# Kernel tuning notes

Measured on AMD Instinct MI355X. Metric: run time of the kernel, lower is better.

Reference implementation:

```python
import jax, jax.numpy as jnp
import numpy as np

N, E = 50000, 800000
IN, H, D, K = 256, 4, 64, 3
NEG_SLOPE = 0.2

def leaky_relu(x):
    return jnp.where(x >= 0, x, NEG_SLOPE * x)

def setup_inputs() -> dict:
    key = jax.random.key(0)
    ks = jax.random.split(key, 10)
    feat = jax.random.normal(ks[0], (N, IN), dtype=jnp.float32)
    src = jax.random.randint(ks[1], (E,), 0, N)
    dst = jax.random.randint(ks[2], (E,), 0, N)
    g = np.sqrt(2.0)  # relu gain used by xavier init; scale irrelevant to math
    W_src = jax.random.normal(ks[3], (H * D, IN), dtype=jnp.float32) * (g * np.sqrt(2.0 / (IN + H * D)))
    attn_l = jax.random.normal(ks[4], (1, H, D), dtype=jnp.float32) * 0.1
    attn_r = jax.random.normal(ks[5], (1, H, D), dtype=jnp.float32) * 0.1
    hop_attn_l = jax.random.normal(ks[6], (1, H, D), dtype=jnp.float32) * 0.1
    hop_attn_r = jax.random.normal(ks[7], (1, H, D), dtype=jnp.float32) * 0.1
    pos_emb = jax.random.normal(ks[8], (1, H, K + 1, D), dtype=jnp.float32) * 0.1
    bias = jnp.zeros((H * D,), dtype=jnp.float32)
    return {"feat": feat, "src": src, "dst": dst, "W_src": W_src,
            "attn_l": attn_l, "attn_r": attn_r, "hop_attn_l": hop_attn_l,
            "hop_attn_r": hop_attn_r, "pos_emb": pos_emb, "bias": bias}

def edge_softmax_dst(e, dst):
    # e: [E, H], softmax over incoming edges of each dst node
    m = jax.ops.segment_max(e, dst, num_segments=N)          # [N, H]
    m = jnp.where(jnp.isfinite(m), m, 0.0)                   # empty segments
    ex = jnp.exp(e - m[dst])                                 # [E, H]
    s = jax.ops.segment_sum(ex, dst, num_segments=N)         # [N, H]
    denom = s[dst]
    return jnp.where(denom > 0, ex / denom, 0.0)

def reference(feat, src, dst, W_src, attn_l, attn_r, hop_attn_l, hop_attn_r, pos_emb, bias):
    # fc_src (shared with fc_dst): [N, IN] -> [N, H, D]
    feat_src = (feat @ W_src.T).reshape(N, H, D)
    feat_dst = feat_src  # share_weights=True
    # GAT transition matrix, norm_by='dst'
    el = jnp.sum(feat_src * attn_l, axis=-1)   # [N, H]
    er = jnp.sum(feat_dst * attn_r, axis=-1)   # [N, H]
    e = leaky_relu(el[src] + er[dst])          # [E, H]
    a = edge_softmax_dst(e, dst)               # [E, H]
    # K-hop diffusion with positional embedding per hop
    h = feat_src
    hstack = [h + pos_emb[:, :, 0, :]]
    for k in range(1, K + 1):
        msg = a[:, :, None] * h[src]                          # [E, H, D]
        h = jax.ops.segment_sum(msg, dst, num_segments=N)     # [N, H, D]
        hstack.append(h + pos_emb[:, :, k, :])
    hs = jnp.stack(hstack, axis=2)                            # [N, H, K+1, D]
    # Hop-wise attention (HA)
    a_l = jnp.sum(hs * hop_attn_l[:, :, None, :], axis=-1, keepdims=True)            # [N,H,K+1,1]
    a_r = jnp.sum(hs[:, :, :1, :] * hop_attn_r[:, :, None, :], axis=-1, keepdims=True)  # [N,H,1,1]
    hop_a = jax.nn.softmax(leaky_relu(a_l + a_r), axis=2)
    rst = jnp.sum(hs * hop_a, axis=2)                         # [N, H, D]
    rst = rst + bias.reshape(1, H, D)
    return rst
```

## Files before the change

### kernel.cpp

```cpp
#include <hip/hip_runtime.h>
#include <hip/hip_bf16.h>
#include <hip/hip_fp16.h>

#define NN 50000
#define EE 800000
#define INF_ 256
#define HH 4
#define DD 64
#define KK 3
#define NEG_SLOPE 0.2f

struct __align__(8) half4 { __half2 a, b; };

__device__ __forceinline__ float lrelu(float x) {
    return x >= 0.0f ? x : NEG_SLOPE * x;
}

__device__ __forceinline__ float wave_sum(float v) {
    #pragma unroll
    for (int m = 1; m < 64; m <<= 1) v += __shfl_xor(v, m, 64);
    return v;
}

__global__ __launch_bounds__(256) void gemm_fs(const float* __restrict__ A,
                                               const float* __restrict__ W,
                                               const float* __restrict__ al,
                                               const float* __restrict__ ar,
                                               float* __restrict__ C,
                                               __half* __restrict__ C16,
                                               float* __restrict__ el,
                                               float* __restrict__ er, int M) {
    const int K = INF_;
    __shared__ float As[16][68];
    __shared__ float Bs[16][68];
    int tid = threadIdx.x;
    int tx = tid & 15, ty = tid >> 4;
    int m0 = blockIdx.y * 64;
    int j0 = blockIdx.x * 64;
    int lrow = tid >> 2;
    int lcol4 = (tid & 3) * 4;
    float c[4][4] = {};
    for (int k0 = 0; k0 < K; k0 += 16) {
        float4 av = make_float4(0.f, 0.f, 0.f, 0.f);
        if (m0 + lrow < M) av = *(const float4*)&A[(size_t)(m0 + lrow) * K + k0 + lcol4];
        float4 bv = *(const float4*)&W[(size_t)(j0 + lrow) * K + k0 + lcol4];
        As[lcol4 + 0][lrow] = av.x; As[lcol4 + 1][lrow] = av.y;
        As[lcol4 + 2][lrow] = av.z; As[lcol4 + 3][lrow] = av.w;
        Bs[lcol4 + 0][lrow] = bv.x; Bs[lcol4 + 1][lrow] = bv.y;
        Bs[lcol4 + 2][lrow] = bv.z; Bs[lcol4 + 3][lrow] = bv.w;
        __syncthreads();
        #pragma unroll
        for (int k = 0; k < 16; ++k) {
            float4 a = *(const float4*)&As[k][ty * 4];
            float4 b = *(const float4*)&Bs[k][tx * 4];
            c[0][0] = fmaf(a.x, b.x, c[0][0]); c[0][1] = fmaf(a.x, b.y, c[0][1]);
            c[0][2] = fmaf(a.x, b.z, c[0][2]); c[0][3] = fmaf(a.x, b.w, c[0][3]);
            c[1][0] = fmaf(a.y, b.x, c[1][0]); c[1][1] = fmaf(a.y, b.y, c[1][1]);
            c[1][2] = fmaf(a.y, b.z, c[1][2]); c[1][3] = fmaf(a.y, b.w, c[1][3]);
            c[2][0] = fmaf(a.z, b.x, c[2][0]); c[2][1] = fmaf(a.z, b.y, c[2][1]);
            c[2][2] = fmaf(a.z, b.z, c[2][2]); c[2][3] = fmaf(a.z, b.w, c[2][3]);
            c[3][0] = fmaf(a.w, b.x, c[3][0]); c[3][1] = fmaf(a.w, b.y, c[3][1]);
            c[3][2] = fmaf(a.w, b.z, c[3][2]); c[3][3] = fmaf(a.w, b.w, c[3][3]);
        }
        __syncthreads();
    }
    #pragma unroll
    for (int i = 0; i < 4; ++i) {
        int m = m0 + ty * 4 + i;
        if (m < M) {
            *(float4*)&C[(size_t)m * 256 + j0 + tx * 4] =
                make_float4(c[i][0], c[i][1], c[i][2], c[i][3]);
            half4 q;
            q.a = __floats2half2_rn(c[i][0], c[i][1]);
            q.b = __floats2half2_rn(c[i][2], c[i][3]);
            *(half4*)&C16[(size_t)m * 256 + j0 + tx * 4] = q;
        }
    }
    float4 al4 = *(const float4*)&al[j0 + tx * 4];
    float4 ar4 = *(const float4*)&ar[j0 + tx * 4];
    float pl[4], pr[4];
    #pragma unroll
    for (int i = 0; i < 4; ++i) {
        pl[i] = c[i][0] * al4.x + c[i][1] * al4.y + c[i][2] * al4.z + c[i][3] * al4.w;
        pr[i] = c[i][0] * ar4.x + c[i][1] * ar4.y + c[i][2] * ar4.z + c[i][3] * ar4.w;
    }
    #pragma unroll
    for (int msk = 1; msk < 16; msk <<= 1) {
        #pragma unroll
        for (int i = 0; i < 4; ++i) {
            pl[i] += __shfl_xor(pl[i], msk, 16);
            pr[i] += __shfl_xor(pr[i], msk, 16);
        }
    }
    if (tx == 0) {
        int h = blockIdx.x;
        #pragma unroll
        for (int i = 0; i < 4; ++i) {
            int m = m0 + ty * 4 + i;
            if (m < M) { el[m * 4 + h] = pl[i]; er[m * 4 + h] = pr[i]; }
        }
    }
}

__global__ void count_k(const int* __restrict__ dst, int* __restrict__ cnt, int E) {
    int e = blockIdx.x * 256 + threadIdx.x;
    if (e < E) atomicAdd(&cnt[dst[e]], 1);
}

__global__ __launch_bounds__(256) void scan1(const int* __restrict__ counts,
                                             int* __restrict__ offs,
                                             int* __restrict__ bsums, int n) {
    __shared__ int sh[256];
    int b = blockIdx.x, t = threadIdx.x;
    int base = b * 1024 + t * 4;
    int v[4];
    #pragma unroll
    for (int i = 0; i < 4; ++i) v[i] = (base + i < n) ? counts[base + i] : 0;
    int tsum = v[0] + v[1] + v[2] + v[3];
    sh[t] = tsum; __syncthreads();
    for (int off = 1; off < 256; off <<= 1) {
        int x = (t >= off) ? sh[t - off] : 0;
        __syncthreads();
        sh[t] += x;
        __syncthreads();
    }
    int run = sh[t] - tsum;
    #pragma unroll
    for (int i = 0; i < 4; ++i) { if (base + i < n) offs[base + i] = run; run += v[i]; }
    if (t == 255) bsums[b] = sh[255];
}

__global__ void scan2(int* bsums, int nb) {
    if (threadIdx.x == 0 && blockIdx.x == 0) {
        int run = 0;
        for (int i = 0; i < nb; ++i) { int v = bsums[i]; bsums[i] = run; run += v; }
    }
}

__global__ __launch_bounds__(256) void scan3(int* __restrict__ offs,
                                             const int* __restrict__ bsums,
                                             int* __restrict__ cursor, int n, int E) {
    int b = blockIdx.x;
    int base = b * 1024 + threadIdx.x * 4;
    int add = bsums[b];
    #pragma unroll
    for (int i = 0; i < 4; ++i) {
        if (base + i < n) {
            int v = offs[base + i] + add;
            offs[base + i] = v;
            cursor[base + i] = v;
        }
    }
    if (b == 0 && threadIdx.x == 0) offs[n] = E;
}

__global__ void scatter_edges(const int* __restrict__ src, const int* __restrict__ dst,
                              const float4* __restrict__ el4, const float4* __restrict__ er4,
                              int* __restrict__ cursor, int* __restrict__ ssrc,
                              float4* __restrict__ alog, int E) {
    int e = blockIdx.x * 256 + threadIdx.x;
    if (e >= E) return;
    int s = src[e], d = dst[e];
    int slot = atomicAdd(&cursor[d], 1);
    ssrc[slot] = s;
    float4 a = el4[s], b = er4[d];
    float4 o;
    o.x = lrelu(a.x + b.x);
    o.y = lrelu(a.y + b.y);
    o.z = lrelu(a.z + b.z);
    o.w = lrelu(a.w + b.w);
    alog[slot] = o;
}

__global__ __launch_bounds__(256) void edge_softmax(const int* __restrict__ offs,
                                                    float* __restrict__ alog, int n) {
    int t = blockIdx.x * 256 + threadIdx.x;
    if (t >= n * 4) return;
    int node = t >> 2, h = t & 3;
    int o0 = offs[node], o1 = offs[node + 1];
    if (o0 >= o1) return;
    float m = -1e30f;
    for (int i = o0; i < o1; ++i) m = fmaxf(m, alog[i * 4 + h]);
    float s = 0.f;
    for (int i = o0; i < o1; ++i) {
        float v = expf(alog[i * 4 + h] - m);
        alog[i * 4 + h] = v;
        s += v;
    }
    float inv = 1.0f / s;
    for (int i = o0; i < o1; ++i) alog[i * 4 + h] *= inv;
}

__global__ __launch_bounds__(256) void hop_kernel(const int* __restrict__ offs,
                                                  const int* __restrict__ ssrc,
                                                  const float* __restrict__ alog,
                                                  const __half* __restrict__ hin,
                                                  __half* __restrict__ hout) {
    int w = threadIdx.x >> 6;
    int n = blockIdx.x * 4 + w;
    if (n >= NN) return;
    int lane = threadIdx.x & 63;
    int h = lane >> 4;
    int col = lane * 4;
    int o0 = offs[n], o1 = offs[n + 1];
    float4 acc0 = make_float4(0.f, 0.f, 0.f, 0.f);
    float4 acc1 = make_float4(0.f, 0.f, 0.f, 0.f);
    float4 acc2 = make_float4(0.f, 0.f, 0.f, 0.f);
    float4 acc3 = make_float4(0.f, 0.f, 0.f, 0.f);
    int i = o0;
    for (; i + 4 <= o1; i += 4) {
        int s0 = ssrc[i], s1 = ssrc[i + 1], s2 = ssrc[i + 2], s3 = ssrc[i + 3];
        float a0 = alog[i * 4 + h];
        float a1 = alog[(i + 1) * 4 + h];
        float a2 = alog[(i + 2) * 4 + h];
        float a3 = alog[(i + 3) * 4 + h];
        half4 v0 = *(const half4*)&hin[(size_t)s0 * 256 + col];
        half4 v1 = *(const half4*)&hin[(size_t)s1 * 256 + col];
        half4 v2 = *(const half4*)&hin[(size_t)s2 * 256 + col];
        half4 v3 = *(const half4*)&hin[(size_t)s3 * 256 + col];
        float2 f0a = __half22float2(v0.a), f0b = __half22float2(v0.b);
        float2 f1a = __half22float2(v1.a), f1b = __half22float2(v1.b);
        float2 f2a = __half22float2(v2.a), f2b = __half22float2(v2.b);
        float2 f3a = __half22float2(v3.a), f3b = __half22float2(v3.b);
        acc0.x = fmaf(a0, f0a.x, acc0.x); acc0.y = fmaf(a0, f0a.y, acc0.y);
        acc0.z = fmaf(a0, f0b.x, acc0.z); acc0.w = fmaf(a0, f0b.y, acc0.w);
        acc1.x = fmaf(a1, f1a.x, acc1.x); acc1.y = fmaf(a1, f1a.y, acc1.y);
        acc1.z = fmaf(a1, f1b.x, acc1.z); acc1.w = fmaf(a1, f1b.y, acc1.w);
        acc2.x = fmaf(a2, f2a.x, acc2.x); acc2.y = fmaf(a2, f2a.y, acc2.y);
        acc2.z = fmaf(a2, f2b.x, acc2.z); acc2.w = fmaf(a2, f2b.y, acc2.w);
        acc3.x = fmaf(a3, f3a.x, acc3.x); acc3.y = fmaf(a3, f3a.y, acc3.y);
        acc3.z = fmaf(a3, f3b.x, acc3.z); acc3.w = fmaf(a3, f3b.y, acc3.w);
    }
    for (; i < o1; ++i) {
        int s0 = ssrc[i];
        float a0 = alog[i * 4 + h];
        half4 v0 = *(const half4*)&hin[(size_t)s0 * 256 + col];
        float2 f0a = __half22float2(v0.a), f0b = __half22float2(v0.b);
        acc0.x = fmaf(a0, f0a.x, acc0.x); acc0.y = fmaf(a0, f0a.y, acc0.y);
        acc0.z = fmaf(a0, f0b.x, acc0.z); acc0.w = fmaf(a0, f0b.y, acc0.w);
    }
    float4 r;
    r.x = (acc0.x + acc1.x) + (acc2.x + acc3.x);
    r.y = (acc0.y + acc1.y) + (acc2.y + acc3.y);
    r.z = (acc0.z + acc1.z) + (acc2.z + acc3.z);
    r.w = (acc0.w + acc1.w) + (acc2.w + acc3.w);
    half4 q;
    q.a = __floats2half2_rn(r.x, r.y);
    q.b = __floats2half2_rn(r.z, r.w);
    *(half4*)&hout[(size_t)n * 256 + col] = q;
}

__global__ __launch_bounds__(256) void hop_attn(const float* __restrict__ h0,
                                                const __half* __restrict__ h1,
                                                const __half* __restrict__ h2,
                                                const __half* __restrict__ h3,
                                                const float* __restrict__ pos,
                                                const float* __restrict__ hl,
                                                const float* __restrict__ hr,
                                                const float* __restrict__ bias,
                                                float* __restrict__ out) {
    int n = blockIdx.x, tid = threadIdx.x;
    int h = tid >> 6, d = tid & 63;
    size_t idx = (size_t)n * 256 + tid;
    float v0 = h0[idx] + pos[(h * 4 + 0) * 64 + d];
    float v1 = __half2float(h1[idx]) + pos[(h * 4 + 1) * 64 + d];
    float v2 = __half2float(h2[idx]) + pos[(h * 4 + 2) * 64 + d];
    float v3 = __half2float(h3[idx]) + pos[(h * 4 + 3) * 64 + d];
    float wl = hl[tid], wr = hr[tid];
    float r0 = wave_sum(v0 * wl);
    float r1 = wave_sum(v1 * wl);
    float r2 = wave_sum(v2 * wl);
    float r3 = wave_sum(v3 * wl);
    float ar = wave_sum(v0 * wr);
    float l0 = lrelu(r0 + ar), l1 = lrelu(r1 + ar), l2 = lrelu(r2 + ar), l3 = lrelu(r3 + ar);
    float mm = fmaxf(fmaxf(l0, l1), fmaxf(l2, l3));
    float e0 = expf(l0 - mm), e1 = expf(l1 - mm), e2 = expf(l2 - mm), e3 = expf(l3 - mm);
    float inv = 1.0f / (e0 + e1 + e2 + e3);
    out[idx] = (v0 * e0 + v1 * e1 + v2 * e2 + v3 * e3) * inv + bias[tid];
}

extern "C" void kernel_launch(void* const* d_in, const int* in_sizes, int n_in,
                              void* d_out, int out_size, void* d_ws, size_t ws_size,
                              hipStream_t stream) {
    const float* feat   = (const float*)d_in[0];
    const int*   src    = (const int*)d_in[1];
    const int*   dst    = (const int*)d_in[2];
    const float* W_src  = (const float*)d_in[3];
    const float* attn_l = (const float*)d_in[4];
    const float* attn_r = (const float*)d_in[5];
    const float* hop_l  = (const float*)d_in[6];
    const float* hop_r  = (const float*)d_in[7];
    const float* pos    = (const float*)d_in[8];
    const float* bias   = (const float*)d_in[9];
    float* out = (float*)d_out;

    char* p = (char*)d_ws;
    auto alloc = [&](size_t bytes) {
        char* r = p;
        p += (bytes + 255) & ~(size_t)255;
        return r;
    };
    float*  fs   = (float*)alloc((size_t)NN * 256 * 4);
    __half* fs16 = (__half*)alloc((size_t)NN * 256 * 2);
    __half* h1   = (__half*)alloc((size_t)NN * 256 * 2);
    __half* h2   = (__half*)alloc((size_t)NN * 256 * 2);
    __half* h3   = (__half*)alloc((size_t)NN * 256 * 2);
    int*   offs = (int*)alloc((size_t)(NN + 1) * 4);
    int*   cnt  = (int*)alloc((size_t)NN * 4);
    int*   cur  = (int*)alloc((size_t)NN * 4);
    int*   bsum = (int*)alloc(256);
    float* el   = (float*)alloc((size_t)NN * 4 * 4);
    float* er   = (float*)alloc((size_t)NN * 4 * 4);
    int*   ssrc = (int*)alloc((size_t)EE * 4);
    float* alog = (float*)alloc((size_t)EE * 4 * 4);

    const int nScan = (NN + 1023) / 1024;

    gemm_fs<<<dim3(4, (NN + 63) / 64), 256, 0, stream>>>(feat, W_src, attn_l, attn_r,
                                                         fs, fs16, el, er, NN);
    hipMemsetAsync(cnt, 0, (size_t)NN * 4, stream);
    count_k<<<(EE + 255) / 256, 256, 0, stream>>>(dst, cnt, EE);
    scan1<<<nScan, 256, 0, stream>>>(cnt, offs, bsum, NN);
    scan2<<<1, 64, 0, stream>>>(bsum, nScan);
    scan3<<<nScan, 256, 0, stream>>>(offs, bsum, cur, NN, EE);
    scatter_edges<<<(EE + 255) / 256, 256, 0, stream>>>(src, dst, (const float4*)el,
                                                        (const float4*)er, cur, ssrc,
                                                        (float4*)alog, EE);
    edge_softmax<<<(NN * 4 + 255) / 256, 256, 0, stream>>>(offs, alog, NN);
    hop_kernel<<<(NN + 3) / 4, 256, 0, stream>>>(offs, ssrc, alog, fs16, h1);
    hop_kernel<<<(NN + 3) / 4, 256, 0, stream>>>(offs, ssrc, alog, h1, h2);
    hop_kernel<<<(NN + 3) / 4, 256, 0, stream>>>(offs, ssrc, alog, h2, h3);
    hop_attn<<<NN, 256, 0, stream>>>(fs, h1, h2, h3, pos, hop_l, hop_r, bias, out);
}
```

Measured before the change: 572.8 us.

## Replace FP32 SIMT GEMM with split-bf16 MFMA GEMM

Replaces the scalar fp32 tiled GEMM that computes feat@W^T with a matrix-core kernel. Both operands are split into high and low bf16 halves and combined with three MFMA products to keep near-fp32 accuracy. Each block now holds a full 64x256 A tile in swizzled LDS and covers all 256 output columns, which removes the fourfold re-reading of A across column blocks. The cost is an extra weight-conversion launch, three times the MFMA work, a large LDS footprint (64 KB) that limits occupancy, and scalar uncoalesced output stores.

```diff
diff --git a/kernel.cpp b/kernel.cpp
--- a/kernel.cpp
+++ b/kernel.cpp
@@ -11,6 +11,10 @@
 #define NEG_SLOPE 0.2f
 
 struct __align__(8) half4 { __half2 a, b; };
+struct __align__(8) short4s { short a, b, c, d; };
+
+using bf16x8 = __attribute__((ext_vector_type(8))) short;
+using f32x4  = __attribute__((ext_vector_type(4))) float;
 
 __device__ __forceinline__ float lrelu(float x) {
     return x >= 0.0f ? x : NEG_SLOPE * x;
@@ -22,84 +26,135 @@
     return v;
 }
 
-__global__ __launch_bounds__(256) void gemm_fs(const float* __restrict__ A,
-                                               const float* __restrict__ W,
-                                               const float* __restrict__ al,
-                                               const float* __restrict__ ar,
-                                               float* __restrict__ C,
-                                               __half* __restrict__ C16,
-                                               float* __restrict__ el,
-                                               float* __restrict__ er, int M) {
-    const int K = INF_;
-    __shared__ float As[16][68];
-    __shared__ float Bs[16][68];
+__device__ __forceinline__ short f2bf(float f) {
+    union { float f; unsigned u; } v; v.f = f;
+    unsigned r = (v.u + 0x7FFFu + ((v.u >> 16) & 1u)) >> 16;
+    return (short)r;
+}
+__device__ __forceinline__ float bf2f(short s) {
+    union { unsigned u; float f; } v; v.u = ((unsigned)(unsigned short)s) << 16;
+    return v.f;
+}
+
+__global__ __launch_bounds__(256) void conv_w(const float* __restrict__ W,
+                                              short* __restrict__ Wh,
+                                              short* __restrict__ Wl) {
+    int i = blockIdx.x * 256 + threadIdx.x;
+    float w = W[i];
+    short h = f2bf(w);
+    Wh[i] = h;
+    Wl[i] = f2bf(w - bf2f(h));
+}
+
+__global__ __launch_bounds__(256) void gemm_mfma(const float* __restrict__ A,
+                                                 const short* __restrict__ Wh,
+                                                 const short* __restrict__ Wl,
+                                                 const float* __restrict__ al,
+                                                 const float* __restrict__ ar,
+                                                 float* __restrict__ C,
+                                                 __half* __restrict__ C16,
+                                                 float* __restrict__ el,
+                                                 float* __restrict__ er, int M) {
+    __shared__ short Ah[64 * 256];
+    __shared__ short Al[64 * 256];
     int tid = threadIdx.x;
-    int tx = tid & 15, ty = tid >> 4;
-    int m0 = blockIdx.y * 64;
-    int j0 = blockIdx.x * 64;
-    int lrow = tid >> 2;
-    int lcol4 = (tid & 3) * 4;
-    float c[4][4] = {};
-    for (int k0 = 0; k0 < K; k0 += 16) {
-        float4 av = make_float4(0.f, 0.f, 0.f, 0.f);
-        if (m0 + lrow < M) av = *(const float4*)&A[(size_t)(m0 + lrow) * K + k0 + lcol4];
-        float4 bv = *(const float4*)&W[(size_t)(j0 + lrow) * K + k0 + lcol4];
-        As[lcol4 + 0][lrow] = av.x; As[lcol4 + 1][lrow] = av.y;
-        As[lcol4 + 2][lrow] = av.z; As[lcol4 + 3][lrow] = av.w;
-        Bs[lcol4 + 0][lrow] = bv.x; Bs[lcol4 + 1][lrow] = bv.y;
-        Bs[lcol4 + 2][lrow] = bv.z; Bs[lcol4 + 3][lrow] = bv.w;
-        __syncthreads();
-        #pragma unroll
-        for (int k = 0; k < 16; ++k) {
-            float4 a = *(const float4*)&As[k][ty * 4];
-            float4 b = *(const float4*)&Bs[k][tx * 4];
-            c[0][0] = fmaf(a.x, b.x, c[0][0]); c[0][1] = fmaf(a.x, b.y, c[0][1]);
-            c[0][2] = fmaf(a.x, b.z, c[0][2]); c[0][3] = fmaf(a.x, b.w, c[0][3]);
-            c[1][0] = fmaf(a.y, b.x, c[1][0]); c[1][1] = fmaf(a.y, b.y, c[1][1]);
-            c[1][2] = fmaf(a.y, b.z, c[1][2]); c[1][3] = fmaf(a.y, b.w, c[1][3]);
-            c[2][0] = fmaf(a.z, b.x, c[2][0]); c[2][1] = fmaf(a.z, b.y, c[2][1]);
-            c[2][2] = fmaf(a.z, b.z, c[2][2]); c[2][3] = fmaf(a.z, b.w, c[2][3]);
-            c[3][0] = fmaf(a.w, b.x, c[3][0]); c[3][1] = fmaf(a.w, b.y, c[3][1]);
-            c[3][2] = fmaf(a.w, b.z, c[3][2]); c[3][3] = fmaf(a.w, b.w, c[3][3]);
-        }
-        __syncthreads();
-    }
-    #pragma unroll
-    for (int i = 0; i < 4; ++i) {
-        int m = m0 + ty * 4 + i;
-        if (m < M) {
-            *(float4*)&C[(size_t)m * 256 + j0 + tx * 4] =
-                make_float4(c[i][0], c[i][1], c[i][2], c[i][3]);
-            half4 q;
-            q.a = __floats2half2_rn(c[i][0], c[i][1]);
-            q.b = __floats2half2_rn(c[i][2], c[i][3]);
-            *(half4*)&C16[(size_t)m * 256 + j0 + tx * 4] = q;
-        }
-    }
-    float4 al4 = *(const float4*)&al[j0 + tx * 4];
-    float4 ar4 = *(const float4*)&ar[j0 + tx * 4];
-    float pl[4], pr[4];
-    #pragma unroll
-    for (int i = 0; i < 4; ++i) {
-        pl[i] = c[i][0] * al4.x + c[i][1] * al4.y + c[i][2] * al4.z + c[i][3] * al4.w;
-        pr[i] = c[i][0] * ar4.x + c[i][1] * ar4.y + c[i][2] * ar4.z + c[i][3] * ar4.w;
-    }
-    #pragma unroll
-    for (int msk = 1; msk < 16; msk <<= 1) {
-        #pragma unroll
-        for (int i = 0; i < 4; ++i) {
-            pl[i] += __shfl_xor(pl[i], msk, 16);
-            pr[i] += __shfl_xor(pr[i], msk, 16);
-        }
-    }
-    if (tx == 0) {
-        int h = blockIdx.x;
-        #pragma unroll
-        for (int i = 0; i < 4; ++i) {
-            int m = m0 + ty * 4 + i;
-            if (m < M) { el[m * 4 + h] = pl[i]; er[m * 4 + h] = pr[i]; }
-        }
-    }
+    int m0 = blockIdx.x * 64;
+
+    {
+        int r4 = tid >> 6;
+        int c4 = (tid & 63) * 4;
+        #pragma unroll
+        for (int it = 0; it < 16; ++it) {
+            int row = it * 4 + r4;
+            int m = m0 + row;
+            float4 v = (m < M) ? *(const float4*)&A[(size_t)m * 256 + c4]
+                               : make_float4(0.f, 0.f, 0.f, 0.f);
+            short h0 = f2bf(v.x), h1 = f2bf(v.y), h2 = f2bf(v.z), h3 = f2bf(v.w);
+            short l0 = f2bf(v.x - bf2f(h0)), l1 = f2bf(v.y - bf2f(h1));
+            short l2 = f2bf(v.z - bf2f(h2)), l3 = f2bf(v.w - bf2f(h3));
+            int cs = c4 ^ ((row & 7) << 3);
+            short4s sh = { h0, h1, h2, h3 };
+            short4s sl = { l0, l1, l2, l3 };
+            *(short4s*)&Ah[row * 256 + cs] = sh;
+            *(short4s*)&Al[row * 256 + cs] = sl;
+        }
+    }
+    __syncthreads();
+
+    int w = tid >> 6;
+    int lane = tid & 63;
+    int lrow = lane & 15;
+    int lk = lane >> 4;
+    int j0 = w * 64;
+
+    f32x4 acc[4][4] = {};
+
+    #pragma unroll
+    for (int kc = 0; kc < 8; ++kc) {
+        int kbase = kc * 32 + lk * 8;
+        bf16x8 bh[4], bl[4], ah[4], alo[4];
+        #pragma unroll
+        for (int tj = 0; tj < 4; ++tj) {
+            int j = j0 + tj * 16 + lrow;
+            bh[tj] = *(const bf16x8*)&Wh[j * 256 + kbase];
+            bl[tj] = *(const bf16x8*)&Wl[j * 256 + kbase];
+        }
+        #pragma unroll
+        for (int tm = 0; tm < 4; ++tm) {
+            int row = tm * 16 + lrow;
+            int ks = kbase ^ ((row & 7) << 3);
+            ah[tm]  = *(const bf16x8*)&Ah[row * 256 + ks];
+            alo[tm] = *(const bf16x8*)&Al[row * 256 + ks];
+        }
+        #pragma unroll
+        for (int tm = 0; tm < 4; ++tm)
+            #pragma unroll
+            for (int tj = 0; tj < 4; ++tj) {
+                acc[tm][tj] = __builtin_amdgcn_mfma_f32_16x16x32_bf16(ah[tm],  bh[tj], acc[tm][tj], 0, 0, 0);
+                acc[tm][tj] = __builtin_amdgcn_mfma_f32_16x16x32_bf16(alo[tm], bh[tj], acc[tm][tj], 0, 0, 0);
+                acc[tm][tj] = __builtin_amdgcn_mfma_f32_16x16x32_bf16(ah[tm],  bl[tj], acc[tm][tj], 0, 0, 0);
+            }
+    }
+
+    #pragma unroll
+    for (int tm = 0; tm < 4; ++tm)
+        #pragma unroll
+        for (int tj = 0; tj < 4; ++tj)
+            #pragma unroll
+            for (int r = 0; r < 4; ++r) {
+                int m = m0 + tm * 16 + lk * 4 + r;
+                if (m < M) {
+                    int j = j0 + tj * 16 + lrow;
+                    float x = acc[tm][tj][r];
+                    C[(size_t)m * 256 + j] = x;
+                    C16[(size_t)m * 256 + j] = __float2half(x);
+                }
+            }
+
+    float alj[4], arj[4];
+    #pragma unroll
+    for (int tj = 0; tj < 4; ++tj) {
+        alj[tj] = al[j0 + tj * 16 + lrow];
+        arj[tj] = ar[j0 + tj * 16 + lrow];
+    }
+    #pragma unroll
+    for (int tm = 0; tm < 4; ++tm)
+        #pragma unroll
+        for (int r = 0; r < 4; ++r) {
+            float pl = acc[tm][0][r] * alj[0] + acc[tm][1][r] * alj[1] +
+                       acc[tm][2][r] * alj[2] + acc[tm][3][r] * alj[3];
+            float pr = acc[tm][0][r] * arj[0] + acc[tm][1][r] * arj[1] +
+                       acc[tm][2][r] * arj[2] + acc[tm][3][r] * arj[3];
+            #pragma unroll
+            for (int msk = 1; msk < 16; msk <<= 1) {
+                pl += __shfl_xor(pl, msk, 64);
+                pr += __shfl_xor(pr, msk, 64);
+            }
+            if (lrow == 0) {
+                int m = m0 + tm * 16 + lk * 4 + r;
+                if (m < M) { el[m * 4 + w] = pl; er[m * 4 + w] = pr; }
+            }
+        }
 }
 
 __global__ void count_k(const int* __restrict__ dst, int* __restrict__ cnt, int E) {
@@ -313,11 +368,14 @@
     float* er   = (float*)alloc((size_t)NN * 4 * 4);
     int*   ssrc = (int*)alloc((size_t)EE * 4);
     float* alog = (float*)alloc((size_t)EE * 4 * 4);
+    short* Wh   = (short*)alloc((size_t)256 * 256 * 2);
+    short* Wl   = (short*)alloc((size_t)256 * 256 * 2);
 
     const int nScan = (NN + 1023) / 1024;
 
-    gemm_fs<<<dim3(4, (NN + 63) / 64), 256, 0, stream>>>(feat, W_src, attn_l, attn_r,
-                                                         fs, fs16, el, er, NN);
+    conv_w<<<256, 256, 0, stream>>>(W_src, Wh, Wl);
+    gemm_mfma<<<(NN + 63) / 64, 256, 0, stream>>>(feat, Wh, Wl, attn_l, attn_r,
+                                                  fs, fs16, el, er, NN);
     hipMemsetAsync(cnt, 0, (size_t)NN * 4, stream);
     count_k<<<(EE + 255) / 256, 256, 0, stream>>>(dst, cnt, EE);
     scan1<<<nScan, 256, 0, stream>>>(cnt, offs, bsum, NN);
```

Result: faster. 529.8 us (-7.5%).
